# Kernel tuning notes

Hardware: AMD Instinct MI355X
Metric: run time of the kernel (lower is better)

The kernel has to match this reference:

```python
import jax, jax.numpy as jnp
import numpy as np

N_NODES, N_EDGES, N_GRAPHS, EMB_DIM, IMG_DIM, N_TYPES = 50000, 800000, 64, 128, 4096, 30


def gcn_conv(x, W, b, row, col, ew, dis, n):
    # PyG GCNConv: x @ W.T, symmetric-normalized weighted aggregation with self-loops, + bias
    xw = x @ W.T                                            # [N, D]
    norm = dis[row] * ew * dis[col]                          # [E]
    agg = jax.ops.segment_sum(norm[:, None] * xw[row], col, num_segments=n)
    agg = agg + (dis * dis)[:, None] * xw                    # self-loop (weight 1) term
    return agg + b


def setup_inputs() -> dict:
    key = jax.random.key(0)
    ks = jax.random.split(key, 20)
    inp = {
        "images": jax.random.normal(ks[0], (N_GRAPHS, IMG_DIM), jnp.float32),
        "node_types": jax.random.randint(ks[1], (N_NODES,), 0, N_TYPES),
        "edge_index": jax.random.randint(ks[2], (2, N_EDGES), 0, N_NODES),
        "edge_attr": jax.random.uniform(ks[3], (N_EDGES,), jnp.float32),
        "batch": jnp.sort(jax.random.randint(ks[4], (N_NODES,), 0, N_GRAPHS)),
    }
    def lin(k, out_d, in_d):
        s = 1.0 / np.sqrt(in_d)
        kw, kb = jax.random.split(k)
        return (jax.random.uniform(kw, (out_d, in_d), jnp.float32, -s, s),
                jax.random.uniform(kb, (out_d,), jnp.float32, -s, s))
    inp["emb_table"] = jax.random.normal(ks[5], (N_TYPES, EMB_DIM), jnp.float32)
    inp["W_img"], inp["b_img"] = lin(ks[6], IMG_DIM, IMG_DIM)      # frozen image backbone head
    inp["W1"], inp["b1"] = lin(ks[7], EMB_DIM, EMB_DIM)
    inp["W2"], inp["b2"] = lin(ks[8], EMB_DIM, EMB_DIM)
    inp["W3"], inp["b3"] = lin(ks[9], EMB_DIM, EMB_DIM)
    inp["Wi"], inp["bi"] = lin(ks[10], EMB_DIM, IMG_DIM)
    inp["Wc"], inp["bc"] = lin(ks[11], EMB_DIM, IMG_DIM + EMB_DIM)
    return inp


def reference(images, node_types, edge_index, edge_attr, batch, emb_table,
              W_img, b_img, W1, b1, W2, b2, W3, b3, Wi, bi, Wc, bc):
    n = node_types.shape[0]
    B = images.shape[0]
    row, col = edge_index[0], edge_index[1]
    # gcn_norm with self-loops (fill value 1): deg at aggregation endpoint (col)
    deg = jax.ops.segment_sum(edge_attr, col, num_segments=n) + 1.0
    dis = jax.lax.rsqrt(deg)
    # frozen image model (linear stand-in for VGG fc head, output dim 4096)
    xi = images @ W_img.T + b_img                           # [B, 4096]
    # encode_images branch
    oi = xi @ Wi.T + bi
    oi = oi / jnp.linalg.norm(oi, axis=1, keepdims=True)
    # encode_images_with_graphs branch
    xg = emb_table[node_types]                              # [N, D]
    xg = jax.nn.relu(gcn_conv(xg, W1, b1, row, col, edge_attr, dis, n))
    xg = jax.nn.relu(gcn_conv(xg, W2, b2, row, col, edge_attr, dis, n))
    xg = gcn_conv(xg, W3, b3, row, col, edge_attr, dis, n)
    cnt = jax.ops.segment_sum(jnp.ones((n,), xg.dtype), batch, num_segments=B)
    pooled = jax.ops.segment_sum(xg, batch, num_segments=B) / jnp.maximum(cnt, 1.0)[:, None]
    oc = jnp.concatenate([xi, pooled], axis=1) @ Wc.T + bc
    oc = oc / jnp.linalg.norm(oc, axis=1, keepdims=True)
    return (oi, oc)
```

## Files before the change

kernel.cpp:

```cpp
#include <hip/hip_runtime.h>
#include <math.h>

#define NN 50000
#define NE 800000
#define NG 64
#define D 128
#define IMG 4096
#define NT 30
#define SCAN_BLOCKS ((NN + 255) / 256)

typedef unsigned int uint;
typedef unsigned short ushort;
typedef __attribute__((ext_vector_type(8))) __bf16 bf16x8;
typedef __attribute__((ext_vector_type(4))) float f32x4;

__device__ __forceinline__ uint bf16rne(float f) {
  uint h = __float_as_uint(f);
  return (h + 0x7fffu + ((h >> 16) & 1u)) >> 16;
}
__device__ __forceinline__ uint pack2bf(float a, float b) {
  return bf16rne(a) | (bf16rne(b) << 16);
}
__device__ __forceinline__ float bflo(uint u) { return __uint_as_float(u << 16); }
__device__ __forceinline__ float bfhi(uint u) { return __uint_as_float(u & 0xffff0000u); }



__global__ void edge_slot(const int* __restrict__ col, int* __restrict__ cnt,
                          int* __restrict__ slot) {
  int e = blockIdx.x * 256 + threadIdx.x;
  if (e < NE) {
    int c = col[e];
    slot[e] = atomicAdd(&cnt[c], 1);
  }
}

__global__ __launch_bounds__(256) void scan_blocks(const int* __restrict__ cnt,
                                                   int* __restrict__ incl,
                                                   int* __restrict__ partial) {
  __shared__ int sd[256];
  int t = threadIdx.x;
  int i = blockIdx.x * 256 + t;
  int v = (i < NN) ? cnt[i] : 0;
  sd[t] = v;
  __syncthreads();
  #pragma unroll
  for (int s = 1; s < 256; s <<= 1) {
    int add = (t >= s) ? sd[t - s] : 0;
    __syncthreads();
    sd[t] += add;
    __syncthreads();
  }
  if (i < NN) incl[i] = sd[t];
  if (t == 255) partial[blockIdx.x] = sd[255];
}

__global__ __launch_bounds__(256) void scan_partials(int* __restrict__ partial, int nb) {
  __shared__ int sd[256];
  int t = threadIdx.x;
  int v = (t < nb) ? partial[t] : 0;
  sd[t] = v;
  __syncthreads();
  #pragma unroll
  for (int s = 1; s < 256; s <<= 1) {
    int add = (t >= s) ? sd[t - s] : 0;
    __syncthreads();
    sd[t] += add;
    __syncthreads();
  }
  if (t < nb) partial[t] = (t == 0) ? 0 : sd[t - 1];
}

__global__ __launch_bounds__(256) void scan_apply(const int* __restrict__ incl,
                                                  const int* __restrict__ partial,
                                                  int* __restrict__ off) {
  int i = blockIdx.x * 256 + threadIdx.x;
  if (i < NN) off[i + 1] = incl[i] + partial[blockIdx.x];
  if (i == 0) off[0] = 0;
}

__global__ void fill_scatter(const int* __restrict__ row, const int* __restrict__ col,
                             const float* __restrict__ ew, const int* __restrict__ off,
                             const int* __restrict__ slot, int2* __restrict__ edge_se) {
  int e = blockIdx.x * 256 + threadIdx.x;
  if (e < NE) {
    int idx = off[col[e]] + slot[e];
    edge_se[idx] = make_int2(row[e], __float_as_int(ew[e]));
  }
}

__global__ __launch_bounds__(256) void deg_csr(const int* __restrict__ off,
                                               const int2* __restrict__ edge_se,
                                               float* __restrict__ dis) {
  int lane = threadIdx.x & 63;
  int sub = lane >> 4, fl = lane & 15;
  int node = (blockIdx.x * 4 + (threadIdx.x >> 6)) * 4 + sub;
  if (node >= NN) return;
  int s = off[node], e = off[node + 1];
  float acc = 0.f;
  for (int j = s + fl; j < e; j += 16) acc += __int_as_float(edge_se[j].y);
  acc += __shfl_xor(acc, 8);
  acc += __shfl_xor(acc, 4);
  acc += __shfl_xor(acc, 2);
  acc += __shfl_xor(acc, 1);
  if (fl == 0) dis[node] = 1.0f / sqrtf(acc + 1.0f);
}

__global__ __launch_bounds__(256) void norm_fill(const int* __restrict__ off,
                                                 const int2* __restrict__ edge_se,
                                                 const float* __restrict__ dis,
                                                 const int* __restrict__ types,
                                                 int* __restrict__ src_s,
                                                 float* __restrict__ norm_s,
                                                 int* __restrict__ styp_s) {
  int lane = threadIdx.x & 63;
  int sub = lane >> 4, fl = lane & 15;
  int node = (blockIdx.x * 4 + (threadIdx.x >> 6)) * 4 + sub;
  if (node >= NN) return;
  int s = off[node], e = off[node + 1];
  float dc = dis[node];
  for (int j = s + fl; j < e; j += 16) {
    int2 se = edge_se[j];
    int sv = se.x;
    src_s[j] = sv;
    norm_s[j] = dis[sv] * __int_as_float(se.y) * dc;
    styp_s[j] = types[sv];
  }
}

__global__ void embw_k(const float* __restrict__ emb, const float* __restrict__ W,
                       float* __restrict__ embW) {
  int tid = blockIdx.x * 256 + threadIdx.x;
  if (tid < NT * D) {
    int t = tid >> 7, n = tid & 127;
    const float* e = emb + (size_t)t * D;
    const float* w = W + (size_t)n * D;
    float acc = 0.f;
    for (int k = 0; k < D; k += 4) {
      float4 ev = *(const float4*)(e + k);
      float4 wv = *(const float4*)(w + k);
      acc += ev.x * wv.x + ev.y * wv.y + ev.z * wv.z + ev.w * wv.w;
    }
    embW[tid] = acc;
  }
}

__global__ void convW2(const float* __restrict__ W2, const float* __restrict__ W3,
                       uint* __restrict__ Wbf2, uint* __restrict__ Wbf3) {
  int idx = blockIdx.x * 256 + threadIdx.x;
  if (idx < 2 * D * 64) {
    const float2* src = (idx < D * 64) ? (const float2*)W2 : (const float2*)W3;
    uint* dst = (idx < D * 64) ? Wbf2 : Wbf3;
    int j = (idx < D * 64) ? idx : idx - D * 64;
    float2 v = src[j];
    dst[j] = pack2bf(v.x, v.y);
  }
}


__global__ __launch_bounds__(256) void lay1_fused(const int* __restrict__ off,
                                                  const int* __restrict__ styp_s,
                                                  const float* __restrict__ norm_s,
                                                  const float* __restrict__ dis,
                                                  const int* __restrict__ types,
                                                  const float* __restrict__ embW,
                                                  const float* __restrict__ b1,
                                                  uint* __restrict__ outbf) {
  __shared__ float sE[NT * D];
  __shared__ float sB[D];
  int t = threadIdx.x;
  for (int i = t; i < NT * D; i += 256) sE[i] = embW[i];
  if (t < D) sB[t] = b1[t];
  __syncthreads();
  int wave = t >> 6, lane = t & 63;
  #pragma unroll
  for (int r = 0; r < 4; r++) {
    int node = blockIdx.x * 16 + wave * 4 + r;
    if (node >= NN) continue;
    float ax = sB[2 * lane], ay = sB[2 * lane + 1];
    int s = off[node], e = off[node + 1];
    int idx = s;
    for (; idx + 4 <= e; idx += 4) {
      int4 st = *(const int4*)(styp_s + idx);
      float4 nm = *(const float4*)(norm_s + idx);
      float2 e0 = *(const float2*)&sE[st.x * D + 2 * lane];
      float2 e1 = *(const float2*)&sE[st.y * D + 2 * lane];
      float2 e2 = *(const float2*)&sE[st.z * D + 2 * lane];
      float2 e3 = *(const float2*)&sE[st.w * D + 2 * lane];
      ax = fmaf(nm.x, e0.x, ax); ay = fmaf(nm.x, e0.y, ay);
      ax = fmaf(nm.y, e1.x, ax); ay = fmaf(nm.y, e1.y, ay);
      ax = fmaf(nm.z, e2.x, ax); ay = fmaf(nm.z, e2.y, ay);
      ax = fmaf(nm.w, e3.x, ax); ay = fmaf(nm.w, e3.y, ay);
    }
    for (; idx < e; idx++) {
      float nm = norm_s[idx];
      float2 ev = *(const float2*)&sE[styp_s[idx] * D + 2 * lane];
      ax = fmaf(nm, ev.x, ax);
      ay = fmaf(nm, ev.y, ay);
    }
    float dd = dis[node];
    dd *= dd;
    float2 es = *(const float2*)&sE[types[node] * D + 2 * lane];
    ax = fmaf(dd, es.x, ax);
    ay = fmaf(dd, es.y, ay);
    ax = fmaxf(ax, 0.f);
    ay = fmaxf(ay, 0.f);
    outbf[(size_t)node * 64 + lane] = pack2bf(ax, ay);
  }
}


__global__ __launch_bounds__(256) void node_gemm_mfma(const uint* __restrict__ Abf,
                                                      const uint* __restrict__ Wbf,
                                                      uint* __restrict__ outbf) {
  __shared__ ushort tile[4][16][136];
  int w = threadIdx.x >> 6, lane = threadIdx.x & 63;
  int quad = lane >> 4;
  int m0 = blockIdx.x * 64 + w * 16;
  int mrow = m0 + (lane & 15);
  int arow = (mrow < NN) ? mrow : 0;
  uint4 afr[4];
  #pragma unroll
  for (int ks = 0; ks < 4; ks++)
    afr[ks] = *(const uint4*)(Abf + (size_t)arow * 64 + ks * 16 + quad * 4);
  f32x4 acc[8] = {};
  #pragma unroll
  for (int nt = 0; nt < 8; nt++) {
    int n = nt * 16 + (lane & 15);
    #pragma unroll
    for (int ks = 0; ks < 4; ks++) {
      union { uint4 u; bf16x8 v; } au, bu;
      au.u = afr[ks];
      bu.u = *(const uint4*)(Wbf + (size_t)n * 64 + ks * 16 + quad * 4);
      acc[nt] = __builtin_amdgcn_mfma_f32_16x16x32_bf16(au.v, bu.v, acc[nt], 0, 0, 0);
    }
  }
  #pragma unroll
  for (int nt = 0; nt < 8; nt++)
    #pragma unroll
    for (int i = 0; i < 4; i++)
      tile[w][quad * 4 + i][nt * 16 + (lane & 15)] = (ushort)bf16rne(acc[nt][i]);
  __builtin_amdgcn_s_waitcnt(0);
  #pragma unroll
  for (int rep = 0; rep < 4; rep++) {
    int r = rep * 4 + quad;
    int j = lane & 15;
    int node = m0 + r;
    if (node < NN) {
      uint4 v = *(const uint4*)&tile[w][r][j * 8];
      *(uint4*)(outbf + (size_t)node * 64 + j * 4) = v;
    }
  }
}


__global__ __launch_bounds__(256) void aggregate2(const uint* __restrict__ xw,
                                                  const int* __restrict__ off,
                                                  const int* __restrict__ src_s,
                                                  const float* __restrict__ norm_s,
                                                  const float* __restrict__ dis,
                                                  const float* __restrict__ bias, int relu,
                                                  uint* __restrict__ outbf,
                                                  float* __restrict__ outf) {
  const uint2* xw2 = (const uint2*)xw;
  int wave = threadIdx.x >> 6;
  int lane = threadIdx.x & 63;
  int half = lane >> 5;
  int fl = lane & 31;
  int node = (blockIdx.x * 4 + wave) * 2 + half;
  if (node >= NN) return;
  float a0 = 0.f, a1 = 0.f, a2 = 0.f, a3 = 0.f;
  int s = off[node], e = off[node + 1];
  int idx = s;
  int astart = (s + 3) & ~3;
  if (astart > e) astart = e;
  for (; idx < astart; idx++) {
    float nm = norm_s[idx];
    uint2 u = xw2[(size_t)src_s[idx] * 32 + fl];
    a0 = fmaf(nm, bflo(u.x), a0);
    a1 = fmaf(nm, bfhi(u.x), a1);
    a2 = fmaf(nm, bflo(u.y), a2);
    a3 = fmaf(nm, bfhi(u.y), a3);
  }
  for (; idx + 8 <= e; idx += 8) {
    int4 sa = *(const int4*)(src_s + idx);
    int4 sb = *(const int4*)(src_s + idx + 4);
    float4 na = *(const float4*)(norm_s + idx);
    float4 nb = *(const float4*)(norm_s + idx + 4);
    uint2 u0 = xw2[(size_t)sa.x * 32 + fl];
    uint2 u1 = xw2[(size_t)sa.y * 32 + fl];
    uint2 u2 = xw2[(size_t)sa.z * 32 + fl];
    uint2 u3 = xw2[(size_t)sa.w * 32 + fl];
    uint2 u4 = xw2[(size_t)sb.x * 32 + fl];
    uint2 u5 = xw2[(size_t)sb.y * 32 + fl];
    uint2 u6 = xw2[(size_t)sb.z * 32 + fl];
    uint2 u7 = xw2[(size_t)sb.w * 32 + fl];
    a0 = fmaf(na.x, bflo(u0.x), a0); a1 = fmaf(na.x, bfhi(u0.x), a1);
    a2 = fmaf(na.x, bflo(u0.y), a2); a3 = fmaf(na.x, bfhi(u0.y), a3);
    a0 = fmaf(na.y, bflo(u1.x), a0); a1 = fmaf(na.y, bfhi(u1.x), a1);
    a2 = fmaf(na.y, bflo(u1.y), a2); a3 = fmaf(na.y, bfhi(u1.y), a3);
    a0 = fmaf(na.z, bflo(u2.x), a0); a1 = fmaf(na.z, bfhi(u2.x), a1);
    a2 = fmaf(na.z, bflo(u2.y), a2); a3 = fmaf(na.z, bfhi(u2.y), a3);
    a0 = fmaf(na.w, bflo(u3.x), a0); a1 = fmaf(na.w, bfhi(u3.x), a1);
    a2 = fmaf(na.w, bflo(u3.y), a2); a3 = fmaf(na.w, bfhi(u3.y), a3);
    a0 = fmaf(nb.x, bflo(u4.x), a0); a1 = fmaf(nb.x, bfhi(u4.x), a1);
    a2 = fmaf(nb.x, bflo(u4.y), a2); a3 = fmaf(nb.x, bfhi(u4.y), a3);
    a0 = fmaf(nb.y, bflo(u5.x), a0); a1 = fmaf(nb.y, bfhi(u5.x), a1);
    a2 = fmaf(nb.y, bflo(u5.y), a2); a3 = fmaf(nb.y, bfhi(u5.y), a3);
    a0 = fmaf(nb.z, bflo(u6.x), a0); a1 = fmaf(nb.z, bfhi(u6.x), a1);
    a2 = fmaf(nb.z, bflo(u6.y), a2); a3 = fmaf(nb.z, bfhi(u6.y), a3);
    a0 = fmaf(nb.w, bflo(u7.x), a0); a1 = fmaf(nb.w, bfhi(u7.x), a1);
    a2 = fmaf(nb.w, bflo(u7.y), a2); a3 = fmaf(nb.w, bfhi(u7.y), a3);
  }
  for (; idx + 4 <= e; idx += 4) {
    int4 sr = *(const int4*)(src_s + idx);
    float4 nm = *(const float4*)(norm_s + idx);
    uint2 u0 = xw2[(size_t)sr.x * 32 + fl];
    uint2 u1 = xw2[(size_t)sr.y * 32 + fl];
    uint2 u2 = xw2[(size_t)sr.z * 32 + fl];
    uint2 u3 = xw2[(size_t)sr.w * 32 + fl];
    a0 = fmaf(nm.x, bflo(u0.x), a0); a1 = fmaf(nm.x, bfhi(u0.x), a1);
    a2 = fmaf(nm.x, bflo(u0.y), a2); a3 = fmaf(nm.x, bfhi(u0.y), a3);
    a0 = fmaf(nm.y, bflo(u1.x), a0); a1 = fmaf(nm.y, bfhi(u1.x), a1);
    a2 = fmaf(nm.y, bflo(u1.y), a2); a3 = fmaf(nm.y, bfhi(u1.y), a3);
    a0 = fmaf(nm.z, bflo(u2.x), a0); a1 = fmaf(nm.z, bfhi(u2.x), a1);
    a2 = fmaf(nm.z, bflo(u2.y), a2); a3 = fmaf(nm.z, bfhi(u2.y), a3);
    a0 = fmaf(nm.w, bflo(u3.x), a0); a1 = fmaf(nm.w, bfhi(u3.x), a1);
    a2 = fmaf(nm.w, bflo(u3.y), a2); a3 = fmaf(nm.w, bfhi(u3.y), a3);
  }
  for (; idx < e; idx++) {
    float nm = norm_s[idx];
    uint2 u = xw2[(size_t)src_s[idx] * 32 + fl];
    a0 = fmaf(nm, bflo(u.x), a0);
    a1 = fmaf(nm, bfhi(u.x), a1);
    a2 = fmaf(nm, bflo(u.y), a2);
    a3 = fmaf(nm, bfhi(u.y), a3);
  }
  float dd = dis[node];
  dd = dd * dd;
  {
    uint2 u = xw2[(size_t)node * 32 + fl];
    a0 = fmaf(dd, bflo(u.x), a0);
    a1 = fmaf(dd, bfhi(u.x), a1);
    a2 = fmaf(dd, bflo(u.y), a2);
    a3 = fmaf(dd, bfhi(u.y), a3);
  }
  float4 b = *(const float4*)(bias + 4 * fl);
  a0 += b.x; a1 += b.y; a2 += b.z; a3 += b.w;
  if (relu) {
    a0 = fmaxf(a0, 0.f);
    a1 = fmaxf(a1, 0.f);
    a2 = fmaxf(a2, 0.f);
    a3 = fmaxf(a3, 0.f);
  }
  if (outbf) {
    uint2 o;
    o.x = pack2bf(a0, a1);
    o.y = pack2bf(a2, a3);
    ((uint2*)outbf)[(size_t)node * 32 + fl] = o;
  } else {
    ((float4*)outf)[(size_t)node * 32 + fl] = make_float4(a0, a1, a2, a3);
  }
}


__global__ void convA(const float* __restrict__ A, uint* __restrict__ Abf) {
  int idx = blockIdx.x * 256 + threadIdx.x;
  if (idx < 64 * IMG / 2) {
    float2 v = ((const float2*)A)[idx];
    Abf[idx] = pack2bf(v.x, v.y);
  }
}

__global__ __launch_bounds__(256) void img_mfma(const uint* __restrict__ Abf,
                                                const float* __restrict__ W,
                                                float* __restrict__ splitbuf) {
  int wv = threadIdx.x >> 6, lane = threadIdx.x & 63;
  int n = blockIdx.x * 64 + wv * 16 + (lane & 15);
  int kq = (lane >> 4) * 8;
  int k0 = blockIdx.y * 512 + kq;
  f32x4 acc[4] = {{0.f, 0.f, 0.f, 0.f}, {0.f, 0.f, 0.f, 0.f},
                  {0.f, 0.f, 0.f, 0.f}, {0.f, 0.f, 0.f, 0.f}};
  const float* wp = W + (size_t)n * IMG + k0;
  const uint* ap = Abf + (size_t)(lane & 15) * (IMG / 2) + k0 / 2;
  for (int ks = 0; ks < 512; ks += 32) {
    float4 w0 = *(const float4*)(wp + ks);
    float4 w1 = *(const float4*)(wp + ks + 4);
    union { uint4 u; bf16x8 v; } bu;
    bu.u.x = pack2bf(w0.x, w0.y);
    bu.u.y = pack2bf(w0.z, w0.w);
    bu.u.z = pack2bf(w1.x, w1.y);
    bu.u.w = pack2bf(w1.z, w1.w);
    #pragma unroll
    for (int mt = 0; mt < 4; mt++) {
      union { uint4 u; bf16x8 v; } au;
      au.u = *(const uint4*)(ap + (size_t)mt * 16 * (IMG / 2) + ks / 2);
      acc[mt] = __builtin_amdgcn_mfma_f32_16x16x32_bf16(au.v, bu.v, acc[mt], 0, 0, 0);
    }
  }
  #pragma unroll
  for (int mt = 0; mt < 4; mt++)
    #pragma unroll
    for (int i = 0; i < 4; i++) {
      int m = mt * 16 + (lane >> 4) * 4 + i;
      splitbuf[((size_t)blockIdx.y * 64 + m) * IMG + n] = acc[mt][i];
    }
}

__global__ __launch_bounds__(256) void img_reduce(const float* __restrict__ splitbuf,
                                                  const float* __restrict__ bias,
                                                  float* __restrict__ xi) {
  int idx = blockIdx.x * 256 + threadIdx.x;
  if (idx < 64 * IMG) {
    float acc = bias[idx & (IMG - 1)];
    #pragma unroll
    for (int s = 0; s < 8; s++) acc += splitbuf[(size_t)s * 64 * IMG + idx];
    xi[idx] = acc;
  }
}


__global__ __launch_bounds__(256) void biasinit(float* __restrict__ out,
                                                const float* __restrict__ bias, int N) {
  int idx = blockIdx.x * 256 + threadIdx.x;
  if (idx < 64 * N) out[idx] = bias[idx % N];
}

__global__ __launch_bounds__(256) void gemm64(const float* __restrict__ A,
                                              const float* __restrict__ W,
                                              float* __restrict__ out, int N, int K,
                                              int kChunk) {
  __shared__ float xs[16][68];
  __shared__ float ws[16][68];
  int t = threadIdx.x;
  int n0 = blockIdx.x * 64;
  int k0 = blockIdx.y * kChunk;
  int kEnd = min(K, k0 + kChunk);
  int tn = t & 15;
  int tm = t >> 4;
  float acc[4][4] = {};
  for (int kt = k0; kt < kEnd; kt += 16) {
    int kc = (t & 3) * 4;
    int rr = t >> 2;
    float4 va = *(const float4*)(A + (size_t)rr * K + kt + kc);
    xs[kc + 0][rr] = va.x; xs[kc + 1][rr] = va.y; xs[kc + 2][rr] = va.z; xs[kc + 3][rr] = va.w;
    float4 vw = *(const float4*)(W + (size_t)(n0 + rr) * K + kt + kc);
    ws[kc + 0][rr] = vw.x; ws[kc + 1][rr] = vw.y; ws[kc + 2][rr] = vw.z; ws[kc + 3][rr] = vw.w;
    __syncthreads();
    #pragma unroll
    for (int k = 0; k < 16; k++) {
      float4 xv = *(const float4*)&xs[k][tm * 4];
      float4 wv = *(const float4*)&ws[k][tn * 4];
      float xm[4] = {xv.x, xv.y, xv.z, xv.w};
      float wn[4] = {wv.x, wv.y, wv.z, wv.w};
      #pragma unroll
      for (int mi = 0; mi < 4; mi++)
        #pragma unroll
        for (int ni = 0; ni < 4; ni++)
          acc[mi][ni] = fmaf(xm[mi], wn[ni], acc[mi][ni]);
    }
    __syncthreads();
  }
  #pragma unroll
  for (int mi = 0; mi < 4; mi++)
    #pragma unroll
    for (int ni = 0; ni < 4; ni++)
      atomicAdd(&out[(size_t)(tm * 4 + mi) * N + n0 + tn * 4 + ni], acc[mi][ni]);
}


__global__ void graph_bounds(const int* __restrict__ batch, int* __restrict__ goff) {
  int g = threadIdx.x;
  if (g <= NG) {
    int lo = 0, hi = NN;
    while (lo < hi) {
      int mid = (lo + hi) >> 1;
      if (batch[mid] < g) lo = mid + 1; else hi = mid;
    }
    goff[g] = lo;
  }
}

__global__ __launch_bounds__(64) void pool_partial_bf(const uint* __restrict__ xb,
                                                      const int* __restrict__ goff,
                                                      float* __restrict__ pooled) {
  int g = blockIdx.x;
  int chunk = blockIdx.y;
  int fl = threadIdx.x;
  int s = goff[g], e = goff[g + 1];
  float ax = 0.f, ay = 0.f;
  for (int i = s + chunk; i < e; i += 8) {
    uint u = xb[(size_t)i * 64 + fl];
    ax += bflo(u);
    ay += bfhi(u);
  }
  atomicAdd(&pooled[g * D + 2 * fl], ax);
  atomicAdd(&pooled[g * D + 2 * fl + 1], ay);
}

__global__ __launch_bounds__(128) void pool_finish(float* __restrict__ pooled,
                                                   const int* __restrict__ goff) {
  int g = blockIdx.x;
  int t = threadIdx.x;
  int c = goff[g + 1] - goff[g];
  pooled[g * D + t] /= fmaxf((float)c, 1.0f);
}

__global__ __launch_bounds__(256) void build_xcat(const float* __restrict__ xi,
                                                  const float* __restrict__ pooled,
                                                  float* __restrict__ xcat) {
  int idx = blockIdx.x * 256 + threadIdx.x;
  if (idx < 64 * 1056) {
    int r = idx / 1056;
    int c = idx % 1056;
    float4 v = (c < 1024) ? ((const float4*)xi)[r * 1024 + c]
                          : ((const float4*)pooled)[r * 32 + (c - 1024)];
    ((float4*)xcat)[idx] = v;
  }
}

__global__ __launch_bounds__(128) void normalize_rows(const float* __restrict__ oi_raw,
                                                      const float* __restrict__ oc_raw,
                                                      float* __restrict__ out) {
  int r = blockIdx.x;
  int t = threadIdx.x;
  const float* src = (r < 64) ? (oi_raw + r * D) : (oc_raw + (r - 64) * D);
  float v = src[t];
  __shared__ float red[128];
  red[t] = v * v;
  __syncthreads();
  for (int s = 64; s > 0; s >>= 1) {
    if (t < s) red[t] += red[t + s];
    __syncthreads();
  }
  out[r * D + t] = v / sqrtf(red[0]);
}


extern "C" void kernel_launch(void* const* d_in, const int* in_sizes, int n_in,
                              void* d_out, int out_size, void* d_ws, size_t ws_size,
                              hipStream_t stream) {
  const float* images = (const float*)d_in[0];
  const int* node_types = (const int*)d_in[1];
  const int* erow = (const int*)d_in[2];
  const int* ecol = erow + NE;
  const float* eattr = (const float*)d_in[3];
  const int* batch = (const int*)d_in[4];
  const float* emb = (const float*)d_in[5];
  const float* W_img = (const float*)d_in[6];
  const float* b_img = (const float*)d_in[7];
  const float* W1 = (const float*)d_in[8];
  const float* b1 = (const float*)d_in[9];
  const float* W2 = (const float*)d_in[10];
  const float* b2 = (const float*)d_in[11];
  const float* W3 = (const float*)d_in[12];
  const float* b3 = (const float*)d_in[13];
  const float* Wi = (const float*)d_in[14];
  const float* bi = (const float*)d_in[15];
  const float* Wc = (const float*)d_in[16];
  const float* bc = (const float*)d_in[17];
  float* out = (float*)d_out;

  char* w = (char*)d_ws;
  auto alloc = [&](size_t bytes) -> void* {
    void* p = (void*)w;
    w += (bytes + 511) & ~(size_t)511;
    return p;
  };
  int* cnt_i = (int*)alloc(NN * 4);
  float* pooled = (float*)alloc(64 * D * 4);
  size_t zero_bytes = (size_t)(w - (char*)d_ws);
  int* csr_off = (int*)alloc((NN + 1) * 4);
  int* goff = (int*)alloc((NG + 1) * 4);
  int* scan_incl = (int*)alloc(NN * 4);
  int* scan_part = (int*)alloc(SCAN_BLOCKS * 4);
  int* slot = (int*)alloc((size_t)NE * 4);
  int2* edge_se = (int2*)alloc((size_t)NE * 8);
  int* src_s = (int*)alloc((size_t)NE * 4);
  float* norm_s = (float*)alloc((size_t)NE * 4);
  int* styp_s = (int*)alloc((size_t)NE * 4);
  float* dis = (float*)alloc(NN * 4);
  float* embW1 = (float*)alloc(NT * D * 4);
  uint* wbf2 = (uint*)alloc(D * 64 * 4);
  uint* wbf3 = (uint*)alloc(D * 64 * 4);
  uint* bufX = (uint*)alloc((size_t)NN * D * 2);
  uint* bufB = (uint*)alloc((size_t)NN * D * 2);
  float* xi = (float*)alloc((size_t)64 * IMG * 4);
  float* xcat = (float*)alloc((size_t)64 * (IMG + D) * 4);
  float* oi_raw = (float*)alloc(64 * D * 4);
  float* oc_raw = (float*)alloc(64 * D * 4);
  uint* imgAbf = (uint*)alloc((size_t)64 * IMG * 2);
  float* splitbuf = (float*)alloc((size_t)8 * 64 * IMG * 4);

  hipMemsetAsync(d_ws, 0, zero_bytes, stream);

  edge_slot<<<NE / 256, 256, 0, stream>>>(ecol, cnt_i, slot);
  scan_blocks<<<SCAN_BLOCKS, 256, 0, stream>>>(cnt_i, scan_incl, scan_part);
  scan_partials<<<1, 256, 0, stream>>>(scan_part, SCAN_BLOCKS);
  scan_apply<<<SCAN_BLOCKS, 256, 0, stream>>>(scan_incl, scan_part, csr_off);
  fill_scatter<<<NE / 256, 256, 0, stream>>>(erow, ecol, eattr, csr_off, slot, edge_se);
  deg_csr<<<(NN + 15) / 16, 256, 0, stream>>>(csr_off, edge_se, dis);
  norm_fill<<<(NN + 15) / 16, 256, 0, stream>>>(csr_off, edge_se, dis, node_types,
                                                src_s, norm_s, styp_s);

  embw_k<<<(NT * D + 255) / 256, 256, 0, stream>>>(emb, W1, embW1);
  lay1_fused<<<(NN + 15) / 16, 256, 0, stream>>>(csr_off, styp_s, norm_s, dis, node_types,
                                                 embW1, b1, bufX);

  convW2<<<(2 * D * 64 + 255) / 256, 256, 0, stream>>>(W2, W3, wbf2, wbf3);
  int gblk = (NN + 63) / 64;
  int ablk = (NN + 7) / 8;
  node_gemm_mfma<<<gblk, 256, 0, stream>>>(bufX, wbf2, bufB);
  aggregate2<<<ablk, 256, 0, stream>>>(bufB, csr_off, src_s, norm_s, dis, b2, 1,
                                       bufX, (float*)0);
  node_gemm_mfma<<<gblk, 256, 0, stream>>>(bufX, wbf3, bufB);
  aggregate2<<<ablk, 256, 0, stream>>>(bufB, csr_off, src_s, norm_s, dis, b3, 0,
                                       bufX, (float*)0);

  graph_bounds<<<1, 128, 0, stream>>>(batch, goff);
  {
    dim3 g(NG, 8);
    pool_partial_bf<<<g, 64, 0, stream>>>(bufX, goff, pooled);
  }
  pool_finish<<<NG, 128, 0, stream>>>(pooled, goff);

  convA<<<(64 * IMG / 2 + 255) / 256, 256, 0, stream>>>(images, imgAbf);
  {
    dim3 g(IMG / 64, 8);
    img_mfma<<<g, 256, 0, stream>>>(imgAbf, W_img, splitbuf);
  }
  img_reduce<<<(64 * IMG + 255) / 256, 256, 0, stream>>>(splitbuf, b_img, xi);

  biasinit<<<(64 * D + 255) / 256, 256, 0, stream>>>(oi_raw, bi, D);
  {
    dim3 g(D / 64, 32);
    gemm64<<<g, 256, 0, stream>>>(xi, Wi, oi_raw, D, IMG, 128);
  }
  build_xcat<<<(64 * 1056 + 255) / 256, 256, 0, stream>>>(xi, pooled, xcat);
  biasinit<<<(64 * D + 255) / 256, 256, 0, stream>>>(oc_raw, bc, D);
  {
    dim3 g(D / 64, 24);
    gemm64<<<g, 256, 0, stream>>>(xcat, Wc, oc_raw, D, IMG + D, 176);
  }
  normalize_rows<<<128, 128, 0, stream>>>(oi_raw, oc_raw, out);
}
```

Measured before the change: 458.3 us.

## Spread CSR-build atomics over 8 sub-counters per node and fuse small launches

Edge counting now hits 8 sub-buckets per destination node (keyed by edge index mod 8), so fewer atomics contend on the same address. The scan runs over the 8x larger array, with a chunked single-block partial scan and a new apply kernel that writes both sub-bucket offsets and CSR offsets. Several tiny kernels are removed: weight prep is merged into one launch, the bias is folded into the gemm64 accumulator init, and the pool mean division moves into build_xcat. The cost is a larger memset and scan (400K entries instead of 50K), plus a serial loop over about 1563 partials inside one block.

```diff
diff --git a/kernel.cpp b/kernel.cpp
--- a/kernel.cpp
+++ b/kernel.cpp
@@ -7,7 +7,8 @@
 #define D 128
 #define IMG 4096
 #define NT 30
-#define SCAN_BLOCKS ((NN + 255) / 256)
+#define NB8 (NN * 8)
+#define SCAN8_BLOCKS ((NB8 + 255) / 256)
 
 typedef unsigned int uint;
 typedef unsigned short ushort;
@@ -26,12 +27,12 @@
 
 
 
-__global__ void edge_slot(const int* __restrict__ col, int* __restrict__ cnt,
+__global__ void edge_slot(const int* __restrict__ col, int* __restrict__ cnt8,
                           int* __restrict__ slot) {
   int e = blockIdx.x * 256 + threadIdx.x;
   if (e < NE) {
     int c = col[e];
-    slot[e] = atomicAdd(&cnt[c], 1);
+    slot[e] = atomicAdd(&cnt8[c * 8 + (e & 7)], 1);
   }
 }
 
@@ -41,7 +42,7 @@
   __shared__ int sd[256];
   int t = threadIdx.x;
   int i = blockIdx.x * 256 + t;
-  int v = (i < NN) ? cnt[i] : 0;
+  int v = (i < NB8) ? cnt[i] : 0;
   sd[t] = v;
   __syncthreads();
   #pragma unroll
@@ -51,40 +52,56 @@
     sd[t] += add;
     __syncthreads();
   }
-  if (i < NN) incl[i] = sd[t];
+  if (i < NB8) incl[i] = sd[t];
   if (t == 255) partial[blockIdx.x] = sd[255];
 }
 
 __global__ __launch_bounds__(256) void scan_partials(int* __restrict__ partial, int nb) {
   __shared__ int sd[256];
+  __shared__ int sbase;
   int t = threadIdx.x;
-  int v = (t < nb) ? partial[t] : 0;
-  sd[t] = v;
+  if (t == 0) sbase = 0;
   __syncthreads();
-  #pragma unroll
-  for (int s = 1; s < 256; s <<= 1) {
-    int add = (t >= s) ? sd[t - s] : 0;
-    __syncthreads();
-    sd[t] += add;
-    __syncthreads();
-  }
-  if (t < nb) partial[t] = (t == 0) ? 0 : sd[t - 1];
-}
-
-__global__ __launch_bounds__(256) void scan_apply(const int* __restrict__ incl,
-                                                  const int* __restrict__ partial,
-                                                  int* __restrict__ off) {
+  for (int chunk = 0; chunk < nb; chunk += 256) {
+    int i = chunk + t;
+    int v = (i < nb) ? partial[i] : 0;
+    sd[t] = v;
+    __syncthreads();
+    #pragma unroll
+    for (int s = 1; s < 256; s <<= 1) {
+      int add = (t >= s) ? sd[t - s] : 0;
+      __syncthreads();
+      sd[t] += add;
+      __syncthreads();
+    }
+    int base = sbase;
+    if (i < nb) partial[i] = base + sd[t] - v;
+    __syncthreads();
+    if (t == 255) sbase = base + sd[255];
+    __syncthreads();
+  }
+}
+
+__global__ __launch_bounds__(256) void scan_apply8(const int* __restrict__ incl,
+                                                   const int* __restrict__ cnt8,
+                                                   const int* __restrict__ partial,
+                                                   int* __restrict__ ex8,
+                                                   int* __restrict__ csr_off) {
   int i = blockIdx.x * 256 + threadIdx.x;
-  if (i < NN) off[i + 1] = incl[i] + partial[blockIdx.x];
-  if (i == 0) off[0] = 0;
+  if (i < NB8) {
+    int ex = incl[i] - cnt8[i] + partial[blockIdx.x];
+    ex8[i] = ex;
+    if ((i & 7) == 0) csr_off[i >> 3] = ex;
+  }
+  if (i == 0) csr_off[NN] = NE;
 }
 
 __global__ void fill_scatter(const int* __restrict__ row, const int* __restrict__ col,
-                             const float* __restrict__ ew, const int* __restrict__ off,
+                             const float* __restrict__ ew, const int* __restrict__ ex8,
                              const int* __restrict__ slot, int2* __restrict__ edge_se) {
   int e = blockIdx.x * 256 + threadIdx.x;
   if (e < NE) {
-    int idx = off[col[e]] + slot[e];
+    int idx = ex8[col[e] * 8 + (e & 7)] + slot[e];
     edge_se[idx] = make_int2(row[e], __float_as_int(ew[e]));
   }
 }
@@ -128,13 +145,18 @@
   }
 }
 
-__global__ void embw_k(const float* __restrict__ emb, const float* __restrict__ W,
-                       float* __restrict__ embW) {
+__global__ __launch_bounds__(256) void prep_weights(const float* __restrict__ emb,
+                                                    const float* __restrict__ W1,
+                                                    float* __restrict__ embW,
+                                                    const float* __restrict__ W2,
+                                                    const float* __restrict__ W3,
+                                                    uint* __restrict__ Wbf2,
+                                                    uint* __restrict__ Wbf3) {
   int tid = blockIdx.x * 256 + threadIdx.x;
   if (tid < NT * D) {
     int t = tid >> 7, n = tid & 127;
     const float* e = emb + (size_t)t * D;
-    const float* w = W + (size_t)n * D;
+    const float* w = W1 + (size_t)n * D;
     float acc = 0.f;
     for (int k = 0; k < D; k += 4) {
       float4 ev = *(const float4*)(e + k);
@@ -142,18 +164,14 @@
       acc += ev.x * wv.x + ev.y * wv.y + ev.z * wv.z + ev.w * wv.w;
     }
     embW[tid] = acc;
-  }
-}
-
-__global__ void convW2(const float* __restrict__ W2, const float* __restrict__ W3,
-                       uint* __restrict__ Wbf2, uint* __restrict__ Wbf3) {
-  int idx = blockIdx.x * 256 + threadIdx.x;
-  if (idx < 2 * D * 64) {
-    const float2* src = (idx < D * 64) ? (const float2*)W2 : (const float2*)W3;
-    uint* dst = (idx < D * 64) ? Wbf2 : Wbf3;
-    int j = (idx < D * 64) ? idx : idx - D * 64;
-    float2 v = src[j];
-    dst[j] = pack2bf(v.x, v.y);
+  } else if (tid < NT * D + D * 64) {
+    int j = tid - NT * D;
+    float2 v = ((const float2*)W2)[j];
+    Wbf2[j] = pack2bf(v.x, v.y);
+  } else if (tid < NT * D + 2 * D * 64) {
+    int j = tid - NT * D - D * 64;
+    float2 v = ((const float2*)W3)[j];
+    Wbf3[j] = pack2bf(v.x, v.y);
   }
 }
 
@@ -420,14 +438,9 @@
 }
 
 
-__global__ __launch_bounds__(256) void biasinit(float* __restrict__ out,
-                                                const float* __restrict__ bias, int N) {
-  int idx = blockIdx.x * 256 + threadIdx.x;
-  if (idx < 64 * N) out[idx] = bias[idx % N];
-}
-
 __global__ __launch_bounds__(256) void gemm64(const float* __restrict__ A,
                                               const float* __restrict__ W,
+                                              const float* __restrict__ bias,
                                               float* __restrict__ out, int N, int K,
                                               int kChunk) {
   __shared__ float xs[16][68];
@@ -439,6 +452,14 @@
   int tn = t & 15;
   int tm = t >> 4;
   float acc[4][4] = {};
+  if (blockIdx.y == 0) {
+    #pragma unroll
+    for (int ni = 0; ni < 4; ni++) {
+      float bv = bias[n0 + tn * 4 + ni];
+      #pragma unroll
+      for (int mi = 0; mi < 4; mi++) acc[mi][ni] = bv;
+    }
+  }
   for (int kt = k0; kt < kEnd; kt += 16) {
     int kc = (t & 3) * 4;
     int rr = t >> 2;
@@ -498,23 +519,22 @@
   atomicAdd(&pooled[g * D + 2 * fl + 1], ay);
 }
 
-__global__ __launch_bounds__(128) void pool_finish(float* __restrict__ pooled,
-                                                   const int* __restrict__ goff) {
-  int g = blockIdx.x;
-  int t = threadIdx.x;
-  int c = goff[g + 1] - goff[g];
-  pooled[g * D + t] /= fmaxf((float)c, 1.0f);
-}
-
 __global__ __launch_bounds__(256) void build_xcat(const float* __restrict__ xi,
                                                   const float* __restrict__ pooled,
+                                                  const int* __restrict__ goff,
                                                   float* __restrict__ xcat) {
   int idx = blockIdx.x * 256 + threadIdx.x;
   if (idx < 64 * 1056) {
     int r = idx / 1056;
     int c = idx % 1056;
-    float4 v = (c < 1024) ? ((const float4*)xi)[r * 1024 + c]
-                          : ((const float4*)pooled)[r * 32 + (c - 1024)];
+    float4 v;
+    if (c < 1024) {
+      v = ((const float4*)xi)[r * 1024 + c];
+    } else {
+      v = ((const float4*)pooled)[r * 32 + (c - 1024)];
+      float inv = 1.0f / fmaxf((float)(goff[r + 1] - goff[r]), 1.0f);
+      v.x *= inv; v.y *= inv; v.z *= inv; v.w *= inv;
+    }
     ((float4*)xcat)[idx] = v;
   }
 }
@@ -567,13 +587,16 @@
     w += (bytes + 511) & ~(size_t)511;
     return p;
   };
-  int* cnt_i = (int*)alloc(NN * 4);
+  int* cnt8 = (int*)alloc((size_t)NB8 * 4);
   float* pooled = (float*)alloc(64 * D * 4);
+  float* oi_raw = (float*)alloc(64 * D * 4);
+  float* oc_raw = (float*)alloc(64 * D * 4);
   size_t zero_bytes = (size_t)(w - (char*)d_ws);
   int* csr_off = (int*)alloc((NN + 1) * 4);
   int* goff = (int*)alloc((NG + 1) * 4);
-  int* scan_incl = (int*)alloc(NN * 4);
-  int* scan_part = (int*)alloc(SCAN_BLOCKS * 4);
+  int* scan_incl = (int*)alloc((size_t)NB8 * 4);
+  int* scan_part = (int*)alloc(SCAN8_BLOCKS * 4);
+  int* ex8 = (int*)alloc((size_t)NB8 * 4);
   int* slot = (int*)alloc((size_t)NE * 4);
   int2* edge_se = (int2*)alloc((size_t)NE * 8);
   int* src_s = (int*)alloc((size_t)NE * 4);
@@ -587,27 +610,25 @@
   uint* bufB = (uint*)alloc((size_t)NN * D * 2);
   float* xi = (float*)alloc((size_t)64 * IMG * 4);
   float* xcat = (float*)alloc((size_t)64 * (IMG + D) * 4);
-  float* oi_raw = (float*)alloc(64 * D * 4);
-  float* oc_raw = (float*)alloc(64 * D * 4);
   uint* imgAbf = (uint*)alloc((size_t)64 * IMG * 2);
   float* splitbuf = (float*)alloc((size_t)8 * 64 * IMG * 4);
 
   hipMemsetAsync(d_ws, 0, zero_bytes, stream);
 
-  edge_slot<<<NE / 256, 256, 0, stream>>>(ecol, cnt_i, slot);
-  scan_blocks<<<SCAN_BLOCKS, 256, 0, stream>>>(cnt_i, scan_incl, scan_part);
-  scan_partials<<<1, 256, 0, stream>>>(scan_part, SCAN_BLOCKS);
-  scan_apply<<<SCAN_BLOCKS, 256, 0, stream>>>(scan_incl, scan_part, csr_off);
-  fill_scatter<<<NE / 256, 256, 0, stream>>>(erow, ecol, eattr, csr_off, slot, edge_se);
+  edge_slot<<<NE / 256, 256, 0, stream>>>(ecol, cnt8, slot);
+  scan_blocks<<<SCAN8_BLOCKS, 256, 0, stream>>>(cnt8, scan_incl, scan_part);
+  scan_partials<<<1, 256, 0, stream>>>(scan_part, SCAN8_BLOCKS);
+  scan_apply8<<<SCAN8_BLOCKS, 256, 0, stream>>>(scan_incl, cnt8, scan_part, ex8, csr_off);
+  fill_scatter<<<NE / 256, 256, 0, stream>>>(erow, ecol, eattr, ex8, slot, edge_se);
   deg_csr<<<(NN + 15) / 16, 256, 0, stream>>>(csr_off, edge_se, dis);
   norm_fill<<<(NN + 15) / 16, 256, 0, stream>>>(csr_off, edge_se, dis, node_types,
                                                 src_s, norm_s, styp_s);
 
-  embw_k<<<(NT * D + 255) / 256, 256, 0, stream>>>(emb, W1, embW1);
+  prep_weights<<<(NT * D + 2 * D * 64 + 255) / 256, 256, 0, stream>>>(
+      emb, W1, embW1, W2, W3, wbf2, wbf3);
   lay1_fused<<<(NN + 15) / 16, 256, 0, stream>>>(csr_off, styp_s, norm_s, dis, node_types,
                                                  embW1, b1, bufX);
 
-  convW2<<<(2 * D * 64 + 255) / 256, 256, 0, stream>>>(W2, W3, wbf2, wbf3);
   int gblk = (NN + 63) / 64;
   int ablk = (NN + 7) / 8;
   node_gemm_mfma<<<gblk, 256, 0, stream>>>(bufX, wbf2, bufB);
@@ -622,7 +643,6 @@
     dim3 g(NG, 8);
     pool_partial_bf<<<g, 64, 0, stream>>>(bufX, goff, pooled);
   }
-  pool_finish<<<NG, 128, 0, stream>>>(pooled, goff);
 
   convA<<<(64 * IMG / 2 + 255) / 256, 256, 0, stream>>>(images, imgAbf);
   {
@@ -631,16 +651,14 @@
   }
   img_reduce<<<(64 * IMG + 255) / 256, 256, 0, stream>>>(splitbuf, b_img, xi);
 
-  biasinit<<<(64 * D + 255) / 256, 256, 0, stream>>>(oi_raw, bi, D);
   {
     dim3 g(D / 64, 32);
-    gemm64<<<g, 256, 0, stream>>>(xi, Wi, oi_raw, D, IMG, 128);
-  }
-  build_xcat<<<(64 * 1056 + 255) / 256, 256, 0, stream>>>(xi, pooled, xcat);
-  biasinit<<<(64 * D + 255) / 256, 256, 0, stream>>>(oc_raw, bc, D);
+    gemm64<<<g, 256, 0, stream>>>(xi, Wi, bi, oi_raw, D, IMG, 128);
+  }
+  build_xcat<<<(64 * 1056 + 255) / 256, 256, 0, stream>>>(xi, pooled, goff, xcat);
   {
     dim3 g(D / 64, 24);
-    gemm64<<<g, 256, 0, stream>>>(xcat, Wc, oc_raw, D, IMG + D, 176);
+    gemm64<<<g, 256, 0, stream>>>(xcat, Wc, bc, oc_raw, D, IMG + D, 176);
   }
   normalize_rows<<<128, 128, 0, stream>>>(oi_raw, oc_raw, out);
 }
```

Measured after the change: 456.2 us. No clear change (-0.4%).
